# Kernel optimization log

Hardware: AMD Instinct MI355X
Metric: run time of the kernel (lower is better)

## Reference

```python
import jax, jax.numpy as jnp
import numpy as np

N_DB = 200000
D_EMB = 512
N_CLASSES = 10
TOP_K = 32


def setup_inputs() -> dict:
    key = jax.random.key(0)
    k1, k2, k3 = jax.random.split(key, 3)
    x = jax.random.normal(k1, (1, D_EMB), dtype=jnp.float32)
    X_emb = jax.random.normal(k2, (N_DB, D_EMB), dtype=jnp.float32)
    X_cls = jax.random.randint(k3, (N_DB,), 0, N_CLASSES, dtype=jnp.int64)
    return {"x": x, "X_emb": X_emb, "X_cls": X_cls, "k": TOP_K}


def reference(x, X_emb, X_cls, k):
    # Original: for each database row, dist = ||emb - x||_2, keep k smallest
    # (sorted ascending by distance). Fused as cdist (single query) + top_k.
    diff = X_emb - x                      # [N, d] (x broadcasts from [1, d])
    dists = jnp.sqrt(jnp.sum(diff * diff, axis=1))  # [N]
    neg_top, idx = jax.lax.top_k(-dists, k)         # smallest k distances
    nbr_emb = X_emb[idx]                  # [k, d]
    nbr_cls = X_cls[idx]                  # [k]
    nbr_dist = -neg_top                   # [k], ascending
    return nbr_emb, nbr_cls, nbr_dist
```

## Files before the change

kernel.cpp:

```cpp
#include <hip/hip_runtime.h>
#include <float.h>
#include <math.h>

#define N_DB   200000
#define D_EMB  512
#define K      32

#define NBLK   512
#define TPB    512
#define WAVES  (TPB / 64)
#define RPB    ((N_DB + NBLK - 1) / NBLK)
#define NCAND  (NBLK * K)

#define TPB2   512
#define WAVES2 (TPB2 / 64)

__global__ __launch_bounds__(TPB) void knn_dist_topk(
    const float* __restrict__ x,
    const float* __restrict__ X_emb,
    float* __restrict__ cand_d,
    int*   __restrict__ cand_i)
{
    __shared__ float xs[D_EMB];
    __shared__ float dists[RPB];
    __shared__ float redv[WAVES];
    __shared__ int   redi[WAVES];

    const int tid  = threadIdx.x;
    const int wid  = tid >> 6;
    const int lane = tid & 63;
    const int base = blockIdx.x * RPB;
    const int rows = min(RPB, N_DB - base);

    for (int i = tid; i < D_EMB; i += TPB) xs[i] = x[i];
    __syncthreads();

    const float4* xq = (const float4*)xs;
    const float4 q0 = xq[lane];
    const float4 q1 = xq[lane + 64];

    const int per_wave = (rows + WAVES - 1) / WAVES;
    const int w0 = min(wid * per_wave, rows);
    const int w1 = min(w0 + per_wave, rows);

    int r = w0;
    for (; r + 4 <= w1; r += 4) {
        const float* rp = X_emb + (size_t)(base + r) * D_EMB;
        const float4* p0 = (const float4*)(rp);
        const float4* p1 = (const float4*)(rp + D_EMB);
        const float4* p2 = (const float4*)(rp + 2 * D_EMB);
        const float4* p3 = (const float4*)(rp + 3 * D_EMB);
        float4 a0 = p0[lane], b0 = p0[lane + 64];
        float4 a1 = p1[lane], b1 = p1[lane + 64];
        float4 a2 = p2[lane], b2 = p2[lane + 64];
        float4 a3 = p3[lane], b3 = p3[lane + 64];
        float s0 = 0.f, s1 = 0.f, s2 = 0.f, s3 = 0.f, d;
        d = a0.x - q0.x; s0 = fmaf(d, d, s0);
        d = a0.y - q0.y; s0 = fmaf(d, d, s0);
        d = a0.z - q0.z; s0 = fmaf(d, d, s0);
        d = a0.w - q0.w; s0 = fmaf(d, d, s0);
        d = b0.x - q1.x; s0 = fmaf(d, d, s0);
        d = b0.y - q1.y; s0 = fmaf(d, d, s0);
        d = b0.z - q1.z; s0 = fmaf(d, d, s0);
        d = b0.w - q1.w; s0 = fmaf(d, d, s0);
        d = a1.x - q0.x; s1 = fmaf(d, d, s1);
        d = a1.y - q0.y; s1 = fmaf(d, d, s1);
        d = a1.z - q0.z; s1 = fmaf(d, d, s1);
        d = a1.w - q0.w; s1 = fmaf(d, d, s1);
        d = b1.x - q1.x; s1 = fmaf(d, d, s1);
        d = b1.y - q1.y; s1 = fmaf(d, d, s1);
        d = b1.z - q1.z; s1 = fmaf(d, d, s1);
        d = b1.w - q1.w; s1 = fmaf(d, d, s1);
        d = a2.x - q0.x; s2 = fmaf(d, d, s2);
        d = a2.y - q0.y; s2 = fmaf(d, d, s2);
        d = a2.z - q0.z; s2 = fmaf(d, d, s2);
        d = a2.w - q0.w; s2 = fmaf(d, d, s2);
        d = b2.x - q1.x; s2 = fmaf(d, d, s2);
        d = b2.y - q1.y; s2 = fmaf(d, d, s2);
        d = b2.z - q1.z; s2 = fmaf(d, d, s2);
        d = b2.w - q1.w; s2 = fmaf(d, d, s2);
        d = a3.x - q0.x; s3 = fmaf(d, d, s3);
        d = a3.y - q0.y; s3 = fmaf(d, d, s3);
        d = a3.z - q0.z; s3 = fmaf(d, d, s3);
        d = a3.w - q0.w; s3 = fmaf(d, d, s3);
        d = b3.x - q1.x; s3 = fmaf(d, d, s3);
        d = b3.y - q1.y; s3 = fmaf(d, d, s3);
        d = b3.z - q1.z; s3 = fmaf(d, d, s3);
        d = b3.w - q1.w; s3 = fmaf(d, d, s3);
        #pragma unroll
        for (int off = 32; off > 0; off >>= 1) {
            s0 += __shfl_xor(s0, off);
            s1 += __shfl_xor(s1, off);
            s2 += __shfl_xor(s2, off);
            s3 += __shfl_xor(s3, off);
        }
        if (lane == 0) {
            dists[r]     = sqrtf(s0);
            dists[r + 1] = sqrtf(s1);
            dists[r + 2] = sqrtf(s2);
            dists[r + 3] = sqrtf(s3);
        }
    }
    for (; r < w1; ++r) {
        const float4* p = (const float4*)(X_emb + (size_t)(base + r) * D_EMB);
        float4 a = p[lane];
        float4 b = p[lane + 64];
        float s = 0.f, d;
        d = a.x - q0.x; s = fmaf(d, d, s);
        d = a.y - q0.y; s = fmaf(d, d, s);
        d = a.z - q0.z; s = fmaf(d, d, s);
        d = a.w - q0.w; s = fmaf(d, d, s);
        d = b.x - q1.x; s = fmaf(d, d, s);
        d = b.y - q1.y; s = fmaf(d, d, s);
        d = b.z - q1.z; s = fmaf(d, d, s);
        d = b.w - q1.w; s = fmaf(d, d, s);
        #pragma unroll
        for (int off = 32; off > 0; off >>= 1) s += __shfl_xor(s, off);
        if (lane == 0) dists[r] = sqrtf(s);
    }
    __syncthreads();

    for (int it = 0; it < K; ++it) {
        float bv = FLT_MAX;
        int   bi = 0x7FFFFFFF;
        for (int i = tid; i < rows; i += TPB) {
            float v = dists[i];
            if (v < bv) { bv = v; bi = i; }
        }
        #pragma unroll
        for (int off = 32; off > 0; off >>= 1) {
            float ov = __shfl_xor(bv, off);
            int   oi = __shfl_xor(bi, off);
            if (ov < bv || (ov == bv && oi < bi)) { bv = ov; bi = oi; }
        }
        if (lane == 0) { redv[wid] = bv; redi[wid] = bi; }
        __syncthreads();
        if (tid == 0) {
            float v = redv[0]; int b = redi[0];
            #pragma unroll
            for (int w = 1; w < WAVES; ++w) {
                if (redv[w] < v || (redv[w] == v && redi[w] < b)) {
                    v = redv[w]; b = redi[w];
                }
            }
            cand_d[blockIdx.x * K + it] = v;
            cand_i[blockIdx.x * K + it] = base + b;
            if (b >= 0 && b < rows) dists[b] = FLT_MAX;
        }
        __syncthreads();
    }
}

__global__ __launch_bounds__(TPB2) void knn_final(
    const float* __restrict__ X_emb,
    const int*   __restrict__ X_cls,
    const float* __restrict__ cand_d,
    const int*   __restrict__ cand_i,
    float* __restrict__ out)
{
    __shared__ float cd[NCAND];
    __shared__ float redv[WAVES2];
    __shared__ int   redi[WAVES2];
    __shared__ int   sel_i[K];
    __shared__ float sel_d[K];

    const int tid  = threadIdx.x;
    const int wid  = tid >> 6;
    const int lane = tid & 63;

    for (int i = tid; i < NCAND; i += TPB2) cd[i] = cand_d[i];
    __syncthreads();

    for (int it = 0; it < K; ++it) {
        float bv = FLT_MAX;
        int   bi = 0x7FFFFFFF;
        for (int i = tid; i < NCAND; i += TPB2) {
            float v = cd[i];
            if (v < bv) { bv = v; bi = i; }
        }
        #pragma unroll
        for (int off = 32; off > 0; off >>= 1) {
            float ov = __shfl_xor(bv, off);
            int   oi = __shfl_xor(bi, off);
            if (ov < bv || (ov == bv && oi < bi)) { bv = ov; bi = oi; }
        }
        if (lane == 0) { redv[wid] = bv; redi[wid] = bi; }
        __syncthreads();
        if (tid == 0) {
            float v = redv[0]; int b = redi[0];
            #pragma unroll
            for (int w = 1; w < WAVES2; ++w) {
                if (redv[w] < v || (redv[w] == v && redi[w] < b)) {
                    v = redv[w]; b = redi[w];
                }
            }
            sel_d[it] = v;
            sel_i[it] = cand_i[b];
            cd[b] = FLT_MAX;
        }
        __syncthreads();
    }

    float4* out_emb = (float4*)out;
    for (int rr = wid; rr < K; rr += WAVES2) {
        const float4* p = (const float4*)(X_emb + (size_t)sel_i[rr] * D_EMB);
        out_emb[rr * 128 + lane]      = p[lane];
        out_emb[rr * 128 + lane + 64] = p[lane + 64];
    }
    if (tid < K) {
        out[K * D_EMB + tid]     = (float)X_cls[sel_i[tid]];
        out[K * D_EMB + K + tid] = sel_d[tid];
    }
}

extern "C" void kernel_launch(void* const* d_in, const int* in_sizes, int n_in,
                              void* d_out, int out_size, void* d_ws, size_t ws_size,
                              hipStream_t stream) {
    const float* x     = (const float*)d_in[0];
    const float* X_emb = (const float*)d_in[1];
    const int*   X_cls = (const int*)d_in[2];

    float* cand_d = (float*)d_ws;
    int*   cand_i = (int*)((char*)d_ws + NCAND * sizeof(float));

    knn_dist_topk<<<NBLK, TPB, 0, stream>>>(x, X_emb, cand_d, cand_i);
    knn_final<<<1, TPB2, 0, stream>>>(X_emb, X_cls, cand_d, cand_i, (float*)d_out);
}
```

Baseline: 671.9 us.

## Replace barrier-based top-k with register-resident wave-level selection and nontemporal loads

Both kernels' block-wide iterative argmin, which took two barriers per selected element, is replaced by single-wave selection over candidates held in registers using shuffle reductions. The final kernel becomes a two-level merge: each wave picks its own top-K, then one wave merges them. Squared distances are kept until the end and sqrt is applied only to the 32 outputs. The embedding stream now uses nontemporal loads to avoid polluting caches. This cuts synchronisation and shared-memory scanning in the selection phase, at the cost of higher register use and leaving 7 of 8 waves idle during per-block selection.

```diff
diff --git a/kernel.cpp b/kernel.cpp
--- a/kernel.cpp
+++ b/kernel.cpp
@@ -10,10 +10,15 @@
 #define TPB    512
 #define WAVES  (TPB / 64)
 #define RPB    ((N_DB + NBLK - 1) / NBLK)
+#define SELREG ((RPB + 63) / 64)
 #define NCAND  (NBLK * K)
 
 #define TPB2   512
 #define WAVES2 (TPB2 / 64)
+#define CPW    (NCAND / WAVES2)
+#define CREG   (CPW / 64)
+
+typedef float v4f __attribute__((ext_vector_type(4)));
 
 __global__ __launch_bounds__(TPB) void knn_dist_topk(
     const float* __restrict__ x,
@@ -23,8 +28,6 @@
 {
     __shared__ float xs[D_EMB];
     __shared__ float dists[RPB];
-    __shared__ float redv[WAVES];
-    __shared__ int   redi[WAVES];
 
     const int tid  = threadIdx.x;
     const int wid  = tid >> 6;
@@ -35,9 +38,9 @@
     for (int i = tid; i < D_EMB; i += TPB) xs[i] = x[i];
     __syncthreads();
 
-    const float4* xq = (const float4*)xs;
-    const float4 q0 = xq[lane];
-    const float4 q1 = xq[lane + 64];
+    const v4f* xq = (const v4f*)xs;
+    const v4f q0 = xq[lane];
+    const v4f q1 = xq[lane + 64];
 
     const int per_wave = (rows + WAVES - 1) / WAVES;
     const int w0 = min(wid * per_wave, rows);
@@ -46,14 +49,18 @@
     int r = w0;
     for (; r + 4 <= w1; r += 4) {
         const float* rp = X_emb + (size_t)(base + r) * D_EMB;
-        const float4* p0 = (const float4*)(rp);
-        const float4* p1 = (const float4*)(rp + D_EMB);
-        const float4* p2 = (const float4*)(rp + 2 * D_EMB);
-        const float4* p3 = (const float4*)(rp + 3 * D_EMB);
-        float4 a0 = p0[lane], b0 = p0[lane + 64];
-        float4 a1 = p1[lane], b1 = p1[lane + 64];
-        float4 a2 = p2[lane], b2 = p2[lane + 64];
-        float4 a3 = p3[lane], b3 = p3[lane + 64];
+        const v4f* p0 = (const v4f*)(rp);
+        const v4f* p1 = (const v4f*)(rp + D_EMB);
+        const v4f* p2 = (const v4f*)(rp + 2 * D_EMB);
+        const v4f* p3 = (const v4f*)(rp + 3 * D_EMB);
+        v4f a0 = __builtin_nontemporal_load(&p0[lane]);
+        v4f b0 = __builtin_nontemporal_load(&p0[lane + 64]);
+        v4f a1 = __builtin_nontemporal_load(&p1[lane]);
+        v4f b1 = __builtin_nontemporal_load(&p1[lane + 64]);
+        v4f a2 = __builtin_nontemporal_load(&p2[lane]);
+        v4f b2 = __builtin_nontemporal_load(&p2[lane + 64]);
+        v4f a3 = __builtin_nontemporal_load(&p3[lane]);
+        v4f b3 = __builtin_nontemporal_load(&p3[lane + 64]);
         float s0 = 0.f, s1 = 0.f, s2 = 0.f, s3 = 0.f, d;
         d = a0.x - q0.x; s0 = fmaf(d, d, s0);
         d = a0.y - q0.y; s0 = fmaf(d, d, s0);
@@ -95,16 +102,16 @@
             s3 += __shfl_xor(s3, off);
         }
         if (lane == 0) {
-            dists[r]     = sqrtf(s0);
-            dists[r + 1] = sqrtf(s1);
-            dists[r + 2] = sqrtf(s2);
-            dists[r + 3] = sqrtf(s3);
+            dists[r]     = s0;
+            dists[r + 1] = s1;
+            dists[r + 2] = s2;
+            dists[r + 3] = s3;
         }
     }
     for (; r < w1; ++r) {
-        const float4* p = (const float4*)(X_emb + (size_t)(base + r) * D_EMB);
-        float4 a = p[lane];
-        float4 b = p[lane + 64];
+        const v4f* p = (const v4f*)(X_emb + (size_t)(base + r) * D_EMB);
+        v4f a = __builtin_nontemporal_load(&p[lane]);
+        v4f b = __builtin_nontemporal_load(&p[lane + 64]);
         float s = 0.f, d;
         d = a.x - q0.x; s = fmaf(d, d, s);
         d = a.y - q0.y; s = fmaf(d, d, s);
@@ -116,38 +123,39 @@
         d = b.w - q1.w; s = fmaf(d, d, s);
         #pragma unroll
         for (int off = 32; off > 0; off >>= 1) s += __shfl_xor(s, off);
-        if (lane == 0) dists[r] = sqrtf(s);
-    }
-    __syncthreads();
-
-    for (int it = 0; it < K; ++it) {
-        float bv = FLT_MAX;
-        int   bi = 0x7FFFFFFF;
-        for (int i = tid; i < rows; i += TPB) {
-            float v = dists[i];
-            if (v < bv) { bv = v; bi = i; }
-        }
-        #pragma unroll
-        for (int off = 32; off > 0; off >>= 1) {
-            float ov = __shfl_xor(bv, off);
-            int   oi = __shfl_xor(bi, off);
-            if (ov < bv || (ov == bv && oi < bi)) { bv = ov; bi = oi; }
-        }
-        if (lane == 0) { redv[wid] = bv; redi[wid] = bi; }
-        __syncthreads();
-        if (tid == 0) {
-            float v = redv[0]; int b = redi[0];
-            #pragma unroll
-            for (int w = 1; w < WAVES; ++w) {
-                if (redv[w] < v || (redv[w] == v && redi[w] < b)) {
-                    v = redv[w]; b = redi[w];
-                }
-            }
-            cand_d[blockIdx.x * K + it] = v;
-            cand_i[blockIdx.x * K + it] = base + b;
-            if (b >= 0 && b < rows) dists[b] = FLT_MAX;
-        }
-        __syncthreads();
+        if (lane == 0) dists[r] = s;
+    }
+    __syncthreads();
+
+    if (wid == 0) {
+        float dv[SELREG];
+        int   di[SELREG];
+        #pragma unroll
+        for (int j = 0; j < SELREG; ++j) {
+            const int idx = j * 64 + lane;
+            dv[j] = (idx < rows) ? dists[idx] : FLT_MAX;
+            di[j] = base + idx;
+        }
+        for (int it = 0; it < K; ++it) {
+            float bv = dv[0];
+            int   bi = di[0];
+            #pragma unroll
+            for (int j = 1; j < SELREG; ++j) {
+                if (dv[j] < bv || (dv[j] == bv && di[j] < bi)) { bv = dv[j]; bi = di[j]; }
+            }
+            #pragma unroll
+            for (int off = 32; off > 0; off >>= 1) {
+                float ov = __shfl_xor(bv, off);
+                int   oi = __shfl_xor(bi, off);
+                if (ov < bv || (ov == bv && oi < bi)) { bv = ov; bi = oi; }
+            }
+            if (lane == 0) {
+                cand_d[blockIdx.x * K + it] = bv;
+                cand_i[blockIdx.x * K + it] = bi;
+            }
+            #pragma unroll
+            for (int j = 0; j < SELREG; ++j) if (di[j] == bi) dv[j] = FLT_MAX;
+        }
     }
 }
 
@@ -158,58 +166,83 @@
     const int*   __restrict__ cand_i,
     float* __restrict__ out)
 {
-    __shared__ float cd[NCAND];
-    __shared__ float redv[WAVES2];
-    __shared__ int   redi[WAVES2];
-    __shared__ int   sel_i[K];
-    __shared__ float sel_d[K];
+    __shared__ float sd[WAVES2 * K];
+    __shared__ int   si[WAVES2 * K];
+    __shared__ float fd[K];
+    __shared__ int   fi[K];
 
     const int tid  = threadIdx.x;
     const int wid  = tid >> 6;
     const int lane = tid & 63;
 
-    for (int i = tid; i < NCAND; i += TPB2) cd[i] = cand_d[i];
-    __syncthreads();
-
-    for (int it = 0; it < K; ++it) {
-        float bv = FLT_MAX;
-        int   bi = 0x7FFFFFFF;
-        for (int i = tid; i < NCAND; i += TPB2) {
-            float v = cd[i];
-            if (v < bv) { bv = v; bi = i; }
-        }
-        #pragma unroll
-        for (int off = 32; off > 0; off >>= 1) {
-            float ov = __shfl_xor(bv, off);
-            int   oi = __shfl_xor(bi, off);
-            if (ov < bv || (ov == bv && oi < bi)) { bv = ov; bi = oi; }
-        }
-        if (lane == 0) { redv[wid] = bv; redi[wid] = bi; }
-        __syncthreads();
-        if (tid == 0) {
-            float v = redv[0]; int b = redi[0];
-            #pragma unroll
-            for (int w = 1; w < WAVES2; ++w) {
-                if (redv[w] < v || (redv[w] == v && redi[w] < b)) {
-                    v = redv[w]; b = redi[w];
-                }
-            }
-            sel_d[it] = v;
-            sel_i[it] = cand_i[b];
-            cd[b] = FLT_MAX;
-        }
-        __syncthreads();
-    }
-
-    float4* out_emb = (float4*)out;
+    {
+        float dv[CREG];
+        int   di[CREG];
+        const int cbase = wid * CPW;
+        #pragma unroll
+        for (int j = 0; j < CREG; ++j) {
+            const int c = cbase + j * 64 + lane;
+            dv[j] = cand_d[c];
+            di[j] = cand_i[c];
+        }
+        for (int it = 0; it < K; ++it) {
+            float bv = dv[0];
+            int   bi = di[0];
+            #pragma unroll
+            for (int j = 1; j < CREG; ++j) {
+                if (dv[j] < bv || (dv[j] == bv && di[j] < bi)) { bv = dv[j]; bi = di[j]; }
+            }
+            #pragma unroll
+            for (int off = 32; off > 0; off >>= 1) {
+                float ov = __shfl_xor(bv, off);
+                int   oi = __shfl_xor(bi, off);
+                if (ov < bv || (ov == bv && oi < bi)) { bv = ov; bi = oi; }
+            }
+            if (lane == 0) { sd[wid * K + it] = bv; si[wid * K + it] = bi; }
+            #pragma unroll
+            for (int j = 0; j < CREG; ++j) if (di[j] == bi) dv[j] = FLT_MAX;
+        }
+    }
+    __syncthreads();
+
+    if (wid == 0) {
+        float ev[4];
+        int   ei[4];
+        #pragma unroll
+        for (int j = 0; j < 4; ++j) {
+            const int idx = j * 64 + lane;
+            ev[j] = sd[idx];
+            ei[j] = si[idx];
+        }
+        for (int it = 0; it < K; ++it) {
+            float bv = ev[0];
+            int   bi = ei[0];
+            #pragma unroll
+            for (int j = 1; j < 4; ++j) {
+                if (ev[j] < bv || (ev[j] == bv && ei[j] < bi)) { bv = ev[j]; bi = ei[j]; }
+            }
+            #pragma unroll
+            for (int off = 32; off > 0; off >>= 1) {
+                float ov = __shfl_xor(bv, off);
+                int   oi = __shfl_xor(bi, off);
+                if (ov < bv || (ov == bv && oi < bi)) { bv = ov; bi = oi; }
+            }
+            if (lane == 0) { fd[it] = sqrtf(bv); fi[it] = bi; }
+            #pragma unroll
+            for (int j = 0; j < 4; ++j) if (ei[j] == bi) ev[j] = FLT_MAX;
+        }
+    }
+    __syncthreads();
+
+    v4f* out_emb = (v4f*)out;
     for (int rr = wid; rr < K; rr += WAVES2) {
-        const float4* p = (const float4*)(X_emb + (size_t)sel_i[rr] * D_EMB);
+        const v4f* p = (const v4f*)(X_emb + (size_t)fi[rr] * D_EMB);
         out_emb[rr * 128 + lane]      = p[lane];
         out_emb[rr * 128 + lane + 64] = p[lane + 64];
     }
     if (tid < K) {
-        out[K * D_EMB + tid]     = (float)X_cls[sel_i[tid]];
-        out[K * D_EMB + K + tid] = sel_d[tid];
+        out[K * D_EMB + tid]     = (float)X_cls[fi[tid]];
+        out[K * D_EMB + K + tid] = fd[tid];
     }
 }
 
```

Measured after the change: 623.0 us. -7.3%, faster.
